# Optimization experiments

Measured on AMD Instinct MI355X. Metric: run time of the kernel, lower is better.

Reference implementation:

```python
import jax, jax.numpy as jnp
import numpy as np
from jax import lax

B, C, H, W = 8, 19, 512, 512
LOW_T, HIGH_T = 100.0, 200.0  # cv2.Canny(img, 100, 200)
MAX_HYST_ITERS = 256          # safety cap on hysteresis fixed-point iterations

_KX = jnp.array([[-1., 0., 1.], [-2., 0., 2.], [-1., 0., 1.]], jnp.float32)
_KY = jnp.array([[-1., -2., -1.], [0., 0., 0.], [1., 2., 1.]], jnp.float32)


def _conv3(x, k):
    # x: [B, H+2, W+2] (already padded), k: [3,3] -> [B, H, W]
    return lax.conv_general_dilated(x[:, None], k[None, None], (1, 1), 'VALID')[:, 0]


def _dilate3(s):
    # 8-connected boolean dilation via 3x3 max window
    return lax.reduce_window(s.astype(jnp.int32), 0, lax.max, (1, 3, 3), (1, 1, 1), 'SAME') > 0


def _canny(img):
    # img: [B, H, W] float values in [0, 255]. Returns float32 edge map in {0,1}.
    b, h, w = img.shape
    pad = jnp.pad(img, ((0, 0), (1, 1), (1, 1)), mode='edge')
    gx = _conv3(pad, _KX)
    gy = _conv3(pad, _KY)
    mag = jnp.abs(gx) + jnp.abs(gy)  # cv2 default L1 gradient magnitude
    ang = jnp.degrees(jnp.arctan2(gy, gx)) % 180.0
    mp = jnp.pad(mag, ((0, 0), (1, 1), (1, 1)))
    nb = lambda dy, dx: mp[:, 1 + dy:1 + dy + h, 1 + dx:1 + dx + w]
    # non-maximum suppression along quantized gradient direction
    d0 = (ang < 22.5) | (ang >= 157.5)
    d45 = (ang >= 22.5) & (ang < 67.5)
    d90 = (ang >= 67.5) & (ang < 112.5)
    keep0 = (mag >= nb(0, 1)) & (mag >= nb(0, -1))
    keep45 = (mag >= nb(-1, 1)) & (mag >= nb(1, -1))
    keep90 = (mag >= nb(1, 0)) & (mag >= nb(-1, 0))
    keep135 = (mag >= nb(-1, -1)) & (mag >= nb(1, 1))
    keep = jnp.where(d0, keep0, jnp.where(d45, keep45, jnp.where(d90, keep90, keep135)))
    strong = keep & (mag > HIGH_T)
    weak = keep & (mag > LOW_T)  # weak includes strong
    # hysteresis: propagate strong labels through weak pixels to fixed point
    def cond(c):
        s, changed, it = c
        return changed & (it < MAX_HYST_ITERS)
    def body(c):
        s, _, it = c
        s2 = (weak & _dilate3(s)) | strong
        return (s2, jnp.any(s2 != s), it + 1)
    edges, _, _ = lax.while_loop(cond, body, (strong, jnp.array(True), jnp.array(0)))
    return edges.astype(jnp.float32)


def setup_inputs() -> dict:
    key = jax.random.key(0)
    k1, k2 = jax.random.split(key)
    pred = jax.random.normal(k1, (B, C, H, W), dtype=jnp.float32)
    labels = jax.random.uniform(k2, (B, H, W), dtype=jnp.float32)
    return {'pred': pred, 'labels': labels}


def reference(pred, labels):
    # pred_convert: per-pixel argmax over channel dim -> class ids [B, H, W]
    cls = jnp.argmax(pred, axis=1)
    # canny(): (img * 255).astype('uint8') -- class ids wrap mod 256
    img_p = ((cls * 255) % 256).astype(jnp.float32)
    # labels in [0,1): uint8 cast truncates toward zero
    img_l = jnp.floor(labels * 255.0)
    ep = _canny(img_p)  # [B, H, W] in {0,1}
    el = _canny(img_l)  # [B, H, W] in {0,1}
    # nn.CrossEntropyLoss() on float target of same shape: input [N=B, C=H, d1=W],
    # target is class probabilities; mean over N and d1.
    logp = jax.nn.log_softmax(ep, axis=1)
    return jnp.mean(jnp.sum(-el * logp, axis=1))
```

## Files before the change

kernel.cpp:

```cpp
#include <hip/hip_runtime.h>
#include <hip/hip_bf16.h>
#include <math.h>

typedef unsigned long long u64;
typedef unsigned char u8;
typedef unsigned short u16;
typedef unsigned int u32;

#define BB 8
#define CC 19
#define HH 512
#define WW 512
#define HWSZ (HH*WW)
#define NIMG 16

__global__ __launch_bounds__(256) void k_pre(const float* __restrict__ pred,
                                             const float* __restrict__ lab,
                                             u8* __restrict__ img,
                                             float* __restrict__ out) {
    int idx = blockIdx.x * 256 + threadIdx.x;
    if (idx == 0) out[0] = 0.0f;
    int p4 = idx * 4;
    int b = p4 / HWSZ;
    int rem = p4 - b * HWSZ;
    const float4* base = (const float4*)(pred + (size_t)b * CC * HWSZ + rem);
    float4 best = base[0];
    int ix = 0, iy = 0, iz = 0, iw = 0;
    for (int c = 1; c < CC; ++c) {
        float4 v = base[(size_t)c * (HWSZ / 4)];
        if (v.x > best.x) { best.x = v.x; ix = c; }
        if (v.y > best.y) { best.y = v.y; iy = c; }
        if (v.z > best.z) { best.z = v.z; iz = c; }
        if (v.w > best.w) { best.w = v.w; iw = c; }
    }
    uchar4 o;
    o.x = (u8)(-ix); o.y = (u8)(-iy); o.z = (u8)(-iz); o.w = (u8)(-iw);
    *(uchar4*)(img + p4) = o;
    float4 v = *(const float4*)(lab + p4);
    uchar4 ol;
    ol.x = (u8)(v.x * 255.0f);
    ol.y = (u8)(v.y * 255.0f);
    ol.z = (u8)(v.z * 255.0f);
    ol.w = (u8)(v.w * 255.0f);
    *(uchar4*)(img + (size_t)BB * HWSZ + p4) = ol;
}

__device__ __forceinline__ void sobel8(const u8* __restrict__ base, int yy, int x0,
                                       int mag8[8], u32* dirpack) {
    int r0 = (yy == 0) ? 0 : yy - 1;
    int r2 = (yy == 511) ? 511 : yy + 1;
    const u8* rps[3] = { base + r0 * WW, base + yy * WW, base + r2 * WW };
    int bb[3][10];
#pragma unroll
    for (int r = 0; r < 3; ++r) {
        u64 m = *(const u64*)(rps[r] + x0);
        bb[r][0] = (x0 == 0) ? rps[r][0] : rps[r][x0 - 1];
#pragma unroll
        for (int i = 0; i < 8; ++i) bb[r][i + 1] = (int)((m >> (8 * i)) & 0xFF);
        bb[r][9] = (x0 == 504) ? rps[r][511] : rps[r][x0 + 8];
    }
    u32 dp = 0;
#pragma unroll
    for (int i = 0; i < 8; ++i) {
        int a00 = bb[0][i], a01 = bb[0][i + 1], a02 = bb[0][i + 2];
        int a10 = bb[1][i],                     a12 = bb[1][i + 2];
        int a20 = bb[2][i], a21 = bb[2][i + 1], a22 = bb[2][i + 2];
        int gx = (a02 + 2 * a12 + a22) - (a00 + 2 * a10 + a20);
        int gy = (a20 + 2 * a21 + a22) - (a00 + 2 * a01 + a02);
        int ax = gx < 0 ? -gx : gx;
        int ay = gy < 0 ? -gy : gy;
        mag8[i] = ax + ay;
        if (dirpack) {
            float fax = (float)ax, fay = (float)ay;
            u32 dir;
            if (fay < 0.41421356237309515f * fax) dir = 0;
            else if (fay >= 2.414213562373095f * fax) dir = 2;
            else dir = ((gx ^ gy) >= 0) ? 1u : 3u;
            dp |= dir << (2 * i);
        }
    }
    if (dirpack) *dirpack = dp;
}

__global__ __launch_bounds__(256) void k_gradnms(const u8* __restrict__ imgs,
                                                 u64* __restrict__ weak,
                                                 u64* __restrict__ strong) {
    __shared__ u16 smag[10][514];
    __shared__ alignas(8) u8 wb[8][64];
    __shared__ alignas(8) u8 sb[8][64];
    int im = blockIdx.x >> 6;
    int y0 = (blockIdx.x & 63) * 8;
    int w    = threadIdx.x >> 6;
    int lane = threadIdx.x & 63;
    int x0 = lane * 8;
    const u8* base = imgs + (size_t)im * HWSZ;

    if (threadIdx.x < 10) { smag[threadIdx.x][0] = 0; smag[threadIdx.x][513] = 0; }

    int ka = 2 * w, kb = 2 * w + 1;
    int mag8a[8], mag8b[8]; u32 dpa, dpb;
    sobel8(base, y0 + ka, x0, mag8a, &dpa);
    sobel8(base, y0 + kb, x0, mag8b, &dpb);
#pragma unroll
    for (int i = 0; i < 8; ++i) smag[ka + 1][1 + x0 + i] = (u16)mag8a[i];
#pragma unroll
    for (int i = 0; i < 8; ++i) smag[kb + 1][1 + x0 + i] = (u16)mag8b[i];

    if (w == 0) {
        if (y0 > 0) {
            int m2[8]; sobel8(base, y0 - 1, x0, m2, nullptr);
#pragma unroll
            for (int i = 0; i < 8; ++i) smag[0][1 + x0 + i] = (u16)m2[i];
        } else {
#pragma unroll
            for (int i = 0; i < 8; ++i) smag[0][1 + x0 + i] = 0;
        }
    } else if (w == 3) {
        if (y0 + 8 < 512) {
            int m2[8]; sobel8(base, y0 + 8, x0, m2, nullptr);
#pragma unroll
            for (int i = 0; i < 8; ++i) smag[9][1 + x0 + i] = (u16)m2[i];
        } else {
#pragma unroll
            for (int i = 0; i < 8; ++i) smag[9][1 + x0 + i] = 0;
        }
    }
    __syncthreads();

#pragma unroll
    for (int rr = 0; rr < 2; ++rr) {
        int k = 2 * w + rr;
        const int* m8 = rr ? mag8b : mag8a;
        u32 dp = rr ? dpb : dpa;
        int wbits = 0, sbits = 0;
#pragma unroll
        for (int i = 0; i < 8; ++i) {
            int x = x0 + i;
            int mag = m8[i];
            int dir = (int)((dp >> (2 * i)) & 3u);
            int n1, n2;
            switch (dir) {
                case 0:  n1 = smag[k + 1][x];     n2 = smag[k + 1][x + 2]; break;
                case 1:  n1 = smag[k][x + 2];     n2 = smag[k + 2][x];     break;
                case 2:  n1 = smag[k][x + 1];     n2 = smag[k + 2][x + 1]; break;
                default: n1 = smag[k][x];         n2 = smag[k + 2][x + 2]; break;
            }
            int keep = (mag >= n1) & (mag >= n2);
            wbits |= (keep & (mag > 100)) << i;
            sbits |= (keep & (mag > 200)) << i;
        }
        wb[k][lane] = (u8)wbits;
        sb[k][lane] = (u8)sbits;
    }
    __syncthreads();

    if (threadIdx.x < 64) {
        int rr = threadIdx.x >> 3;
        int wd = threadIdx.x & 7;
        u64 W = *(const u64*)&wb[rr][wd * 8];
        u64 S = *(const u64*)&sb[rr][wd * 8];
        size_t o = ((size_t)im * HH + (y0 + rr)) * 8 + wd;
        weak[o] = W;
        strong[o] = S;
    }
}

__global__ __launch_bounds__(512) void k_hyst(const u64* __restrict__ weakg,
                                              const u64* __restrict__ strongg,
                                              u64* __restrict__ edges) {
    __shared__ u32 hlo[8][512];
    __shared__ u32 hhi[8][512];
    __shared__ int flags[2];
    int y = threadIdx.x;
    int im = blockIdx.x;
    size_t base = ((size_t)im * HH + y) * 8;
    u64 wk[8], s[8];
#pragma unroll
    for (int j = 0; j < 8; ++j) {
        wk[j] = weakg[base + j];
        s[j] = strongg[base + j];
    }
    for (int it = 0; it < 256; ++it) {
        u64 diff = 0;
        u64 c = 0;
#pragma unroll
        for (int j = 0; j < 8; ++j) {
            u64 a = s[j], w = wk[j];
            u64 t1 = a + w;       u64 c1 = (u64)(t1 < a);
            u64 t2 = t1 + c;      u64 c2 = (u64)(t2 < t1);
            u64 ns = a | ((t2 ^ w) & w);
            diff |= ns ^ a;
            s[j] = ns;
            c = c1 | c2;
        }
        c = 0;
#pragma unroll
        for (int j = 7; j >= 0; --j) {
            u64 a = __builtin_bitreverse64(s[j]);
            u64 w = __builtin_bitreverse64(wk[j]);
            u64 t1 = a + w;       u64 c1 = (u64)(t1 < a);
            u64 t2 = t1 + c;      u64 c2 = (u64)(t2 < t1);
            u64 nsr = a | ((t2 ^ w) & w);
            u64 ns = __builtin_bitreverse64(nsr);
            diff |= ns ^ s[j];
            s[j] = ns;
            c = c1 | c2;
        }
        u64 hh[8];
#pragma unroll
        for (int j = 0; j < 8; ++j) hh[j] = s[j] | (s[j] << 1) | (s[j] >> 1);
#pragma unroll
        for (int j = 1; j < 8; ++j) hh[j] |= s[j - 1] >> 63;
#pragma unroll
        for (int j = 0; j < 7; ++j) hh[j] |= s[j + 1] << 63;
#pragma unroll
        for (int j = 0; j < 8; ++j) {
            hlo[j][y] = (u32)hh[j];
            hhi[j][y] = (u32)(hh[j] >> 32);
        }
        if (y == 0 && it == 0) flags[0] = 0;
        __syncthreads();
        if (y == 0) flags[(it + 1) & 1] = 0;
#pragma unroll
        for (int j = 0; j < 8; ++j) {
            u64 up = (y > 0)   ? ((u64)hlo[j][y - 1] | ((u64)hhi[j][y - 1] << 32)) : 0ull;
            u64 dn = (y < 511) ? ((u64)hlo[j][y + 1] | ((u64)hhi[j][y + 1] << 32)) : 0ull;
            u64 t = wk[j] & (up | dn) & ~s[j];
            diff |= t;
            s[j] |= t;
        }
        if (diff) flags[it & 1] = 1;
        __syncthreads();
        if (!flags[it & 1]) break;
    }
#pragma unroll
    for (int j = 0; j < 8; ++j) edges[base + j] = s[j];
}

__device__ __forceinline__ void tile_transpose64(u64& xr, int lane) {
    u64 x = xr;
#pragma unroll
    for (int k = 0; k < 6; ++k) {
        const int d = 1 << k;
        const u64 m = (k == 0) ? 0x5555555555555555ull :
                      (k == 1) ? 0x3333333333333333ull :
                      (k == 2) ? 0x0F0F0F0F0F0F0F0Full :
                      (k == 3) ? 0x00FF00FF00FF00FFull :
                      (k == 4) ? 0x0000FFFF0000FFFFull :
                                 0x00000000FFFFFFFFull;
        u64 p = (u64)__shfl_xor(x, d, 64);
        u64 tl = ((x >> d) ^ p) & m;
        u64 th = ((p >> d) ^ x) & m;
        x = (lane & d) ? (x ^ th) : (x ^ (tl << d));
    }
    xr = x;
}

__global__ __launch_bounds__(256) void k_loss(const u64* __restrict__ edges,
                                              float* __restrict__ out) {
    int b = blockIdx.x >> 3;
    int j = blockIdx.x & 7;
    int w = threadIdx.x >> 6;
    int lane = threadIdx.x & 63;
    const u64* ep = edges + ((size_t)b * HH) * 8 + j;
    const u64* el = edges + ((size_t)(b + 8) * HH) * 8 + j;
    int k = 0, es = 0, ov = 0;
#pragma unroll
    for (int t = 0; t < 2; ++t) {
        int yb = (2 * w + t) * 64 + lane;
        u64 vp = ep[(size_t)yb * 8];
        u64 vl = el[(size_t)yb * 8];
        tile_transpose64(vp, lane);
        tile_transpose64(vl, lane);
        k  += __popcll(vp);
        es += __popcll(vl);
        ov += __popcll(vp & vl);
    }
    __shared__ int red[3][4][64];
    red[0][w][lane] = k;
    red[1][w][lane] = es;
    red[2][w][lane] = ov;
    __syncthreads();
    if (threadIdx.x < 64) {
        int l = threadIdx.x;
        int K = red[0][0][l] + red[0][1][l] + red[0][2][l] + red[0][3][l];
        int E = red[1][0][l] + red[1][1][l] + red[1][2][l] + red[1][3][l];
        int O = red[2][0][l] + red[2][1][l] + red[2][2][l] + red[2][3][l];
        float logZ = logf(512.0f + 1.7182818284590452f * (float)K);
        float v = ((float)E * logZ - (float)O) * (1.0f / 4096.0f);
#pragma unroll
        for (int o = 32; o > 0; o >>= 1) v += __shfl_down(v, o, 64);
        if (l == 0) atomicAdd(out, v);
    }
}

extern "C" void kernel_launch(void* const* d_in, const int* in_sizes, int n_in,
                              void* d_out, int out_size, void* d_ws, size_t ws_size,
                              hipStream_t stream) {
    const float* pred = (const float*)d_in[0];
    const float* labels = (const float*)d_in[1];
    float* out = (float*)d_out;

    u8*  imgs   = (u8*)d_ws;
    u64* weak   = (u64*)((char*)d_ws + (size_t)NIMG * HWSZ);
    u64* strong = (u64*)((char*)weak + (size_t)NIMG * HH * 8 * 8);
    u64* edges  = (u64*)((char*)strong + (size_t)NIMG * HH * 8 * 8);

    hipLaunchKernelGGL(k_pre, dim3(BB * HWSZ / 4 / 256), dim3(256), 0, stream,
                       pred, labels, imgs, out);
    hipLaunchKernelGGL(k_gradnms, dim3(NIMG * 64), dim3(256), 0, stream,
                       imgs, weak, strong);
    hipLaunchKernelGGL(k_hyst, dim3(NIMG), dim3(512), 0, stream,
                       weak, strong, edges);
    hipLaunchKernelGGL(k_loss, dim3(64), dim3(256), 0, stream, edges, out);
}
```

Measured before the change: 245.4 us.

## Interleave cheap vertical-only hysteresis hops between full passes; nontemporal argmax loads

Restructures the hysteresis loop so that each full pass (horizontal carry-propagation plus vertical step) is followed by up to three cheap vertical-only hops. These hops reuse the dilated rows in shared memory and only recompute them for rows that changed. This is meant to cut the per-iteration ALU cost and converge vertical chains with fewer expensive passes. The pre-pass also switches the argmax and label loads to nontemporal loads so streaming data does not pollute the cache. The two-barrier-per-hop structure and the flag double-buffering add synchronisation complexity and a risk of subtle convergence bugs.

```diff
diff --git a/kernel.cpp b/kernel.cpp
--- a/kernel.cpp
+++ b/kernel.cpp
@@ -6,6 +6,7 @@
 typedef unsigned char u8;
 typedef unsigned short u16;
 typedef unsigned int u32;
+typedef float f32x4 __attribute__((ext_vector_type(4)));
 
 #define BB 8
 #define CC 19
@@ -23,11 +24,11 @@
     int p4 = idx * 4;
     int b = p4 / HWSZ;
     int rem = p4 - b * HWSZ;
-    const float4* base = (const float4*)(pred + (size_t)b * CC * HWSZ + rem);
-    float4 best = base[0];
+    const f32x4* base = (const f32x4*)(pred + (size_t)b * CC * HWSZ + rem);
+    f32x4 best = __builtin_nontemporal_load(&base[0]);
     int ix = 0, iy = 0, iz = 0, iw = 0;
     for (int c = 1; c < CC; ++c) {
-        float4 v = base[(size_t)c * (HWSZ / 4)];
+        f32x4 v = __builtin_nontemporal_load(&base[(size_t)c * (HWSZ / 4)]);
         if (v.x > best.x) { best.x = v.x; ix = c; }
         if (v.y > best.y) { best.y = v.y; iy = c; }
         if (v.z > best.z) { best.z = v.z; iz = c; }
@@ -36,7 +37,7 @@
     uchar4 o;
     o.x = (u8)(-ix); o.y = (u8)(-iy); o.z = (u8)(-iz); o.w = (u8)(-iw);
     *(uchar4*)(img + p4) = o;
-    float4 v = *(const float4*)(lab + p4);
+    f32x4 v = __builtin_nontemporal_load((const f32x4*)(lab + p4));
     uchar4 ol;
     ol.x = (u8)(v.x * 255.0f);
     ol.y = (u8)(v.y * 255.0f);
@@ -165,6 +166,95 @@
     }
 }
 
+__device__ __forceinline__ void hdilate(const u64 s[8], u64 hh[8]) {
+#pragma unroll
+    for (int j = 0; j < 8; ++j) hh[j] = s[j] | (s[j] << 1) | (s[j] >> 1);
+#pragma unroll
+    for (int j = 1; j < 8; ++j) hh[j] |= s[j - 1] >> 63;
+#pragma unroll
+    for (int j = 0; j < 7; ++j) hh[j] |= s[j + 1] << 63;
+}
+
+__device__ __forceinline__ int full_pass(u64 s[8], const u64 wk[8],
+                                         u32 lo[8][512], u32 hi[8][512],
+                                         int* flags, int y, int pc) {
+    u64 diff = 0;
+    u64 c = 0;
+#pragma unroll
+    for (int j = 0; j < 8; ++j) {
+        u64 a = s[j], w = wk[j];
+        u64 t1 = a + w;       u64 c1 = (u64)(t1 < a);
+        u64 t2 = t1 + c;      u64 c2 = (u64)(t2 < t1);
+        u64 ns = a | ((t2 ^ w) & w);
+        diff |= ns ^ a;
+        s[j] = ns;
+        c = c1 | c2;
+    }
+    c = 0;
+#pragma unroll
+    for (int j = 7; j >= 0; --j) {
+        u64 a = __builtin_bitreverse64(s[j]);
+        u64 w = __builtin_bitreverse64(wk[j]);
+        u64 t1 = a + w;       u64 c1 = (u64)(t1 < a);
+        u64 t2 = t1 + c;      u64 c2 = (u64)(t2 < t1);
+        u64 nsr = a | ((t2 ^ w) & w);
+        u64 ns = __builtin_bitreverse64(nsr);
+        diff |= ns ^ s[j];
+        s[j] = ns;
+        c = c1 | c2;
+    }
+    u64 hh[8];
+    hdilate(s, hh);
+#pragma unroll
+    for (int j = 0; j < 8; ++j) { lo[j][y] = (u32)hh[j]; hi[j][y] = (u32)(hh[j] >> 32); }
+    __syncthreads();
+    if (y == 0) flags[(pc + 1) & 1] = 0;
+    u64 hdiff = 0;
+#pragma unroll
+    for (int j = 0; j < 8; ++j) {
+        u64 up = (y > 0)   ? ((u64)lo[j][y - 1] | ((u64)hi[j][y - 1] << 32)) : 0ull;
+        u64 dn = (y < 511) ? ((u64)lo[j][y + 1] | ((u64)hi[j][y + 1] << 32)) : 0ull;
+        u64 t = wk[j] & (up | dn) & ~s[j];
+        hdiff |= t;
+        s[j] |= t;
+    }
+    diff |= hdiff;
+    if (hdiff) {
+        hdilate(s, hh);
+#pragma unroll
+        for (int j = 0; j < 8; ++j) { lo[j][y] = (u32)hh[j]; hi[j][y] = (u32)(hh[j] >> 32); }
+    }
+    if (diff) flags[pc & 1] = 1;
+    __syncthreads();
+    return flags[pc & 1];
+}
+
+__device__ __forceinline__ int vhop(u64 s[8], const u64 wk[8],
+                                    u32 lo[8][512], u32 hi[8][512],
+                                    int* flags, int y, int pc) {
+    u64 t[8]; u64 diff = 0;
+#pragma unroll
+    for (int j = 0; j < 8; ++j) {
+        u64 up = (y > 0)   ? ((u64)lo[j][y - 1] | ((u64)hi[j][y - 1] << 32)) : 0ull;
+        u64 dn = (y < 511) ? ((u64)lo[j][y + 1] | ((u64)hi[j][y + 1] << 32)) : 0ull;
+        t[j] = wk[j] & (up | dn) & ~s[j];
+        diff |= t[j];
+    }
+    __syncthreads();
+    if (y == 0) flags[(pc + 1) & 1] = 0;
+    if (diff) {
+        flags[pc & 1] = 1;
+#pragma unroll
+        for (int j = 0; j < 8; ++j) s[j] |= t[j];
+        u64 hh[8];
+        hdilate(s, hh);
+#pragma unroll
+        for (int j = 0; j < 8; ++j) { lo[j][y] = (u32)hh[j]; hi[j][y] = (u32)(hh[j] >> 32); }
+    }
+    __syncthreads();
+    return flags[pc & 1];
+}
+
 __global__ __launch_bounds__(512) void k_hyst(const u64* __restrict__ weakg,
                                               const u64* __restrict__ strongg,
                                               u64* __restrict__ edges) {
@@ -180,58 +270,13 @@
         wk[j] = weakg[base + j];
         s[j] = strongg[base + j];
     }
+    if (y == 0) flags[0] = 0;
+    int pc = 0;
     for (int it = 0; it < 256; ++it) {
-        u64 diff = 0;
-        u64 c = 0;
-#pragma unroll
-        for (int j = 0; j < 8; ++j) {
-            u64 a = s[j], w = wk[j];
-            u64 t1 = a + w;       u64 c1 = (u64)(t1 < a);
-            u64 t2 = t1 + c;      u64 c2 = (u64)(t2 < t1);
-            u64 ns = a | ((t2 ^ w) & w);
-            diff |= ns ^ a;
-            s[j] = ns;
-            c = c1 | c2;
-        }
-        c = 0;
-#pragma unroll
-        for (int j = 7; j >= 0; --j) {
-            u64 a = __builtin_bitreverse64(s[j]);
-            u64 w = __builtin_bitreverse64(wk[j]);
-            u64 t1 = a + w;       u64 c1 = (u64)(t1 < a);
-            u64 t2 = t1 + c;      u64 c2 = (u64)(t2 < t1);
-            u64 nsr = a | ((t2 ^ w) & w);
-            u64 ns = __builtin_bitreverse64(nsr);
-            diff |= ns ^ s[j];
-            s[j] = ns;
-            c = c1 | c2;
-        }
-        u64 hh[8];
-#pragma unroll
-        for (int j = 0; j < 8; ++j) hh[j] = s[j] | (s[j] << 1) | (s[j] >> 1);
-#pragma unroll
-        for (int j = 1; j < 8; ++j) hh[j] |= s[j - 1] >> 63;
-#pragma unroll
-        for (int j = 0; j < 7; ++j) hh[j] |= s[j + 1] << 63;
-#pragma unroll
-        for (int j = 0; j < 8; ++j) {
-            hlo[j][y] = (u32)hh[j];
-            hhi[j][y] = (u32)(hh[j] >> 32);
-        }
-        if (y == 0 && it == 0) flags[0] = 0;
-        __syncthreads();
-        if (y == 0) flags[(it + 1) & 1] = 0;
-#pragma unroll
-        for (int j = 0; j < 8; ++j) {
-            u64 up = (y > 0)   ? ((u64)hlo[j][y - 1] | ((u64)hhi[j][y - 1] << 32)) : 0ull;
-            u64 dn = (y < 511) ? ((u64)hlo[j][y + 1] | ((u64)hhi[j][y + 1] << 32)) : 0ull;
-            u64 t = wk[j] & (up | dn) & ~s[j];
-            diff |= t;
-            s[j] |= t;
-        }
-        if (diff) flags[it & 1] = 1;
-        __syncthreads();
-        if (!flags[it & 1]) break;
+        if (!full_pass(s, wk, hlo, hhi, flags, y, pc++)) break;
+#pragma unroll 1
+        for (int v = 0; v < 3; ++v)
+            if (!vhop(s, wk, hlo, hhi, flags, y, pc++)) break;
     }
 #pragma unroll
     for (int j = 0; j < 8; ++j) edges[base + j] = s[j];
```

New measurement: 234.6 us. 4.4% less time.
